# Performance work log

Measured on AMD Instinct MI355X. Metric: run time of the kernel, lower is better.

## Reference

```python
import jax, jax.numpy as jnp
import numpy as np

N_NODES = 100000
N_EDGES = 1600000
IN_DIM, HID_DIM, OUT_DIM = 128, 128, 1


def gcn_conv(x, W, b, src, dst, n_nodes):
    """PyG-style GCNConv: add self-loops, symmetric D^-1/2 (A+I) D^-1/2 normalization.

    x: [N, F_in], W: [F_in, F_out], b: [F_out], src/dst: [E] int edge endpoints.
    """
    h = x @ W  # [N, F_out] transform first (as PyG does)
    # degree on A + I, counted over destination (symmetric graph assumption)
    ones = jnp.ones(src.shape[0], dtype=h.dtype)
    deg = jax.ops.segment_sum(ones, dst, num_segments=n_nodes) + 1.0  # +1 self loop
    dinv = jax.lax.rsqrt(deg)  # [N]
    norm = dinv[src] * dinv[dst]  # [E] edge normalization
    msg = h[src] * norm[:, None]  # [E, F_out] gather + scale
    agg = jax.ops.segment_sum(msg, dst, num_segments=n_nodes)  # scatter-add
    # self-loop contribution: norm_ii = dinv[i]^2
    out = agg + h * (dinv * dinv)[:, None]
    return out + b


def setup_inputs() -> dict:
    key = jax.random.key(0)
    k1, k2, k3, k4 = jax.random.split(key, 4)
    x = jax.random.normal(k1, (N_NODES, IN_DIM), dtype=jnp.float32)
    edge_index = jax.random.randint(k2, (2, N_EDGES), 0, N_NODES, dtype=jnp.int64)
    W1 = jax.random.normal(k3, (IN_DIM, HID_DIM), dtype=jnp.float32) * (1.0 / np.sqrt(IN_DIM))
    b1 = jnp.zeros((HID_DIM,), dtype=jnp.float32)
    W2 = jax.random.normal(k4, (HID_DIM, OUT_DIM), dtype=jnp.float32) * (1.0 / np.sqrt(HID_DIM))
    b2 = jnp.zeros((OUT_DIM,), dtype=jnp.float32)
    return {"x": x, "edge_index": edge_index, "W1": W1, "b1": b1, "W2": W2, "b2": b2}


def reference(x, edge_index, W1, b1, W2, b2):
    n = x.shape[0]
    src, dst = edge_index[0], edge_index[1]
    h = gcn_conv(x, W1, b1, src, dst, n)
    h = jax.nn.relu(h)
    # dropout(p=0.2) is identity at inference
    out = gcn_conv(h, W2, b2, src, dst, n)  # [N, 1]
    return out
```

## Files before the change

kernel.cpp:

```cpp
#include <hip/hip_runtime.h>

#define N_NODES 100000
#define N_EDGES 1600000
#define DIM 128

#define BSHIFT 8
#define BNODES 256
#define NBUCK 391
#define BCAP  4608
#define PCHUNK 4096
#define NB_PART ((N_EDGES + PCHUNK - 1) / PCHUNK)

#define GTILES 1563

#define HALF_ELEMS ((size_t)N_NODES * 64)

typedef short s16x8 __attribute__((ext_vector_type(8)));
typedef float f32x4 __attribute__((ext_vector_type(4)));

__device__ __forceinline__ unsigned short f2bf(float f) {
    unsigned u = __float_as_uint(f);
    u += 0x7fffu + ((u >> 16) & 1u);
    return (unsigned short)(u >> 16);
}
__device__ __forceinline__ float bflo(unsigned u) { return __uint_as_float(u << 16); }
__device__ __forceinline__ float bfhi(unsigned u) { return __uint_as_float(u & 0xffff0000u); }

__device__ __forceinline__ void acc8(float (&a)[8], uint4 v, float w) {
    a[0] = fmaf(bflo(v.x), w, a[0]); a[1] = fmaf(bfhi(v.x), w, a[1]);
    a[2] = fmaf(bflo(v.y), w, a[2]); a[3] = fmaf(bfhi(v.y), w, a[3]);
    a[4] = fmaf(bflo(v.z), w, a[4]); a[5] = fmaf(bfhi(v.z), w, a[5]);
    a[6] = fmaf(bflo(v.w), w, a[6]); a[7] = fmaf(bfhi(v.w), w, a[7]);
}


__global__ void k_zero(int* __restrict__ gcur) {
    int t = blockIdx.x * blockDim.x + threadIdx.x;
    if (t < NBUCK) gcur[t] = t * BCAP;
}

__device__ __forceinline__ void part_body(char* smem, int bid,
                                          const int* __restrict__ src,
                                          const int* __restrict__ dst,
                                          int* __restrict__ gcur,
                                          int* __restrict__ ebuf) {
    int* hist = (int*)smem;
    int* gbase = hist + NBUCK;
    int tid = threadIdx.x;
    long e0 = (long)bid * PCHUNK;
    int n = min(PCHUNK, (int)(N_EDGES - e0));
    for (int b = tid; b < NBUCK; b += 256) hist[b] = 0;
    __syncthreads();

    int pk[16], mybk[16];
#pragma unroll
    for (int k = 0; k < 16; ++k) {
        int idx = k * 256 + tid;
        if (idx < n) {
            int s = src[e0 + idx], d = dst[e0 + idx];
            mybk[k] = d >> BSHIFT;
            pk[k] = (s << 8) | (d & 255);
            atomicAdd(&hist[mybk[k]], 1);
        } else {
            mybk[k] = -1;
        }
    }
    __syncthreads();
    for (int b = tid; b < NBUCK; b += 256) {
        gbase[b] = hist[b] ? atomicAdd(&gcur[b], hist[b]) : 0;
        hist[b] = 0;
    }
    __syncthreads();
#pragma unroll
    for (int k = 0; k < 16; ++k) {
        if (mybk[k] >= 0) {
            int b = mybk[k];
            int slot = gbase[b] + atomicAdd(&hist[b], 1);
            ebuf[slot] = pk[k];
        }
    }
}

__device__ __forceinline__ void csr_body(char* smem, int b,
                                         const int* __restrict__ ebuf,
                                         const int* __restrict__ gcur,
                                         int* __restrict__ rp,
                                         int* __restrict__ cnt,
                                         float* __restrict__ dinv,
                                         int* __restrict__ csrs) {
    int* lcnt = (int*)smem;
    int* lcur = lcnt + BNODES;
    int t = threadIdx.x;
    int node0 = b << BSHIFT;
    lcnt[t] = 0;
    __syncthreads();
    int base = b * BCAP, end = gcur[b];
    for (int e = base + t; e < end; e += 256)
        atomicAdd(&lcnt[ebuf[e] & 255], 1);
    __syncthreads();
    int c = lcnt[t];
    lcur[t] = c;
    __syncthreads();
    for (int s = 1; s < 256; s <<= 1) {
        int u = (t >= s) ? lcur[t - s] : 0;
        __syncthreads();
        lcur[t] += u;
        __syncthreads();
    }
    int excl = lcur[t] - c;
    lcur[t] = excl;
    int node = node0 + t;
    if (node < N_NODES) {
        rp[node] = base + excl;
        cnt[node] = c;
        dinv[node] = rsqrtf((float)(c + 1));
    }
    __syncthreads();
    for (int e = base + t; e < end; e += 256) {
        int pkd = ebuf[e];
        int p = atomicAdd(&lcur[pkd & 255], 1);
        csrs[base + p] = (int)((unsigned)pkd >> 8);
    }
}

__device__ __forceinline__ void gemm_body(char* smem, int tile,
                                          const float* __restrict__ x,
                                          const float* __restrict__ W1,
                                          unsigned short* __restrict__ h1h) {
    if (tile >= GTILES) return;
    unsigned short* Wt = (unsigned short*)smem;
    int tid = threadIdx.x;
    for (int idx = tid; idx < DIM * DIM; idx += 256) {
        int k = idx >> 7, c = idx & 127;
        Wt[c * 128 + (k ^ ((c & 7) << 3))] = f2bf(W1[idx]);
    }
    __syncthreads();

    int wv = tid >> 6, lane = tid & 63;
    int g = lane >> 4, tl = lane & 15;
    unsigned short* cst = (unsigned short*)(smem + 32768 + wv * 4096);

    int rb = tile * 64 + wv * 16;
    if (rb >= N_NODES) return;

    s16x8 afrag[4];
    const float* xrow = x + (size_t)(rb + tl) * DIM + g * 8;
#pragma unroll
    for (int kc = 0; kc < 4; ++kc) {
        float4 p0 = *(const float4*)(xrow + kc * 32);
        float4 p1 = *(const float4*)(xrow + kc * 32 + 4);
        s16x8 a;
        a[0] = (short)f2bf(p0.x); a[1] = (short)f2bf(p0.y);
        a[2] = (short)f2bf(p0.z); a[3] = (short)f2bf(p0.w);
        a[4] = (short)f2bf(p1.x); a[5] = (short)f2bf(p1.y);
        a[6] = (short)f2bf(p1.z); a[7] = (short)f2bf(p1.w);
        afrag[kc] = a;
    }

    f32x4 acc[8];
#pragma unroll
    for (int ct = 0; ct < 8; ++ct) acc[ct] = (f32x4)0.0f;
#pragma unroll
    for (int kc = 0; kc < 4; ++kc) {
#pragma unroll
        for (int ct = 0; ct < 8; ++ct) {
            int crow = ct * 16 + tl;
            int boff = crow * 256 + ((kc * 64 + g * 16) ^ ((crow & 7) << 4));
            s16x8 b = *(const s16x8*)((const char*)Wt + boff);
            acc[ct] = __builtin_amdgcn_mfma_f32_16x16x32_bf16(afrag[kc], b, acc[ct], 0, 0, 0);
        }
    }

#pragma unroll
    for (int ct = 0; ct < 8; ++ct) {
#pragma unroll
        for (int r = 0; r < 4; ++r) {
            float own = acc[ct][r];
            float oth = __shfl_xor(own, 1, 64);
            if ((lane & 1) == 0) {
                unsigned pk = (unsigned)f2bf(own) | ((unsigned)f2bf(oth) << 16);
                int row = g * 4 + r;
                int col = ct * 16 + tl;
                *(unsigned*)&cst[row * 128 + (col ^ (row << 3))] = pk;
            }
        }
    }
    asm volatile("s_waitcnt lgkmcnt(0)" ::: "memory");

    int hf = tl >> 3, ch = (tl & 7) * 8;
#pragma unroll
    for (int c = 0; c < 4; ++c) {
        int row = c * 4 + g;
        uint4 v = *(const uint4*)&cst[row * 128 + ((tl ^ row) * 8)];
        *(uint4*)(h1h + (size_t)hf * HALF_ELEMS + (size_t)(rb + row) * 64 + ch) = v;
    }
}

__global__ __launch_bounds__(256) void k_part(const int* __restrict__ src,
                                              const int* __restrict__ dst,
                                              int* __restrict__ gcur,
                                              int* __restrict__ ebuf) {
    __shared__ __align__(16) char smem[2 * NBUCK * 4 + 16];
    part_body(smem, blockIdx.x, src, dst, gcur, ebuf);
}

__global__ __launch_bounds__(256) void k_gemm(const float* __restrict__ x,
                                              const float* __restrict__ W1,
                                              unsigned short* __restrict__ h1h) {
    __shared__ __align__(16) char smem[49152];
    gemm_body(smem, blockIdx.x, x, W1, h1h);
}

__global__ __launch_bounds__(256) void k_csrk(const int* __restrict__ ebuf,
                                              const int* __restrict__ gcur,
                                              int* __restrict__ rp,
                                              int* __restrict__ cnt,
                                              float* __restrict__ dinv,
                                              int* __restrict__ csrs) {
    __shared__ __align__(16) char smem[2 * BNODES * 4];
    csr_body(smem, blockIdx.x, ebuf, gcur, rp, cnt, dinv, csrs);
}

__global__ __launch_bounds__(256) void k_pg(const int* __restrict__ src,
                                            const int* __restrict__ dst,
                                            int* __restrict__ gcur,
                                            int* __restrict__ ebuf,
                                            const float* __restrict__ x,
                                            const float* __restrict__ W1,
                                            unsigned short* __restrict__ h1h) {
    __shared__ __align__(16) char smem[49152];
    if (blockIdx.x < NB_PART) part_body(smem, blockIdx.x, src, dst, gcur, ebuf);
    else                      gemm_body(smem, blockIdx.x - NB_PART, x, W1, h1h);
}


__global__ __launch_bounds__(256) void k_agg1h(const unsigned short* __restrict__ h1h,
                                               const float* __restrict__ dinv,
                                               const int* __restrict__ rp,
                                               const int* __restrict__ cnt,
                                               const int* __restrict__ csrs,
                                               const float* __restrict__ b1,
                                               const float* __restrict__ W2,
                                               float* __restrict__ zpart) {
    int half = blockIdx.x & 1;
    int nb = blockIdx.x >> 1;
    int lane = threadIdx.x & 63;
    int wv = threadIdx.x >> 6;
    int g = lane >> 3, tl = lane & 7;
    int i = nb * 32 + wv * 8 + g;
    int c0 = tl * 8;
    const unsigned short* hbase = h1h + (size_t)half * HALF_ELEMS + c0;
    float di = dinv[i];
    int beg = rp[i], end = beg + cnt[i];
    float a[8];
#pragma unroll
    for (int q = 0; q < 8; ++q) a[q] = 0.f;

    int j = beg;
    for (; j + 4 <= end; j += 4) {
        int s0 = csrs[j], s1 = csrs[j + 1], s2 = csrs[j + 2], s3 = csrs[j + 3];
        uint4 v0 = *(const uint4*)(hbase + (size_t)s0 * 64);
        uint4 v1 = *(const uint4*)(hbase + (size_t)s1 * 64);
        uint4 v2 = *(const uint4*)(hbase + (size_t)s2 * 64);
        uint4 v3 = *(const uint4*)(hbase + (size_t)s3 * 64);
        float w0 = dinv[s0] * di, w1 = dinv[s1] * di;
        float w2 = dinv[s2] * di, w3 = dinv[s3] * di;
        acc8(a, v0, w0);
        acc8(a, v1, w1);
        acc8(a, v2, w2);
        acc8(a, v3, w3);
    }
    for (; j < end; ++j) {
        int s0 = csrs[j];
        uint4 v0 = *(const uint4*)(hbase + (size_t)s0 * 64);
        acc8(a, v0, dinv[s0] * di);
    }

    uint4 vs = *(const uint4*)(hbase + (size_t)i * 64);
    float sii = di * di;
    int cb = half * 64 + c0;
    float4 bA = *(const float4*)(b1 + cb);
    float4 bB = *(const float4*)(b1 + cb + 4);
    float4 wA = *(const float4*)(W2 + cb);
    float4 wB = *(const float4*)(W2 + cb + 4);
    float p = 0.f;
    p += fmaxf(fmaf(bflo(vs.x), sii, a[0]) + bA.x, 0.f) * wA.x;
    p += fmaxf(fmaf(bfhi(vs.x), sii, a[1]) + bA.y, 0.f) * wA.y;
    p += fmaxf(fmaf(bflo(vs.y), sii, a[2]) + bA.z, 0.f) * wA.z;
    p += fmaxf(fmaf(bfhi(vs.y), sii, a[3]) + bA.w, 0.f) * wA.w;
    p += fmaxf(fmaf(bflo(vs.z), sii, a[4]) + bB.x, 0.f) * wB.x;
    p += fmaxf(fmaf(bfhi(vs.z), sii, a[5]) + bB.y, 0.f) * wB.y;
    p += fmaxf(fmaf(bflo(vs.w), sii, a[6]) + bB.z, 0.f) * wB.z;
    p += fmaxf(fmaf(bfhi(vs.w), sii, a[7]) + bB.w, 0.f) * wB.w;
#pragma unroll
    for (int off = 4; off >= 1; off >>= 1) p += __shfl_xor(p, off, 64);
    if (tl == 0) zpart[(size_t)half * N_NODES + i] = p;
}


__global__ __launch_bounds__(256) void k_agg2(const float* __restrict__ zpart,
                                              const float* __restrict__ dinv,
                                              const int* __restrict__ rp,
                                              const int* __restrict__ cnt,
                                              const int* __restrict__ csrs,
                                              const float* __restrict__ b2,
                                              float* __restrict__ out) {
    int grp = threadIdx.x >> 2, r = threadIdx.x & 3;
    int i = blockIdx.x * 64 + grp;
    if (i >= N_NODES) return;
    float di = dinv[i];
    int beg = rp[i], end = beg + cnt[i];
    float acc = 0.f;
    for (int j = beg + r; j < end; j += 4) {
        int s = csrs[j];
        float zs = zpart[s] + zpart[N_NODES + s];
        acc = fmaf(zs, dinv[s] * di, acc);
    }
    acc += __shfl_xor(acc, 1, 64);
    acc += __shfl_xor(acc, 2, 64);
    if (r == 0) {
        float zi = zpart[i] + zpart[N_NODES + i];
        out[i] = acc + zi * di * di + b2[0];
    }
}


extern "C" void kernel_launch(void* const* d_in, const int* in_sizes, int n_in,
                              void* d_out, int out_size, void* d_ws, size_t ws_size,
                              hipStream_t stream) {
    const float* x  = (const float*)d_in[0];
    const int*   ei = (const int*)d_in[1];
    const float* W1 = (const float*)d_in[2];
    const float* b1 = (const float*)d_in[3];
    const float* W2 = (const float*)d_in[4];
    const float* b2 = (const float*)d_in[5];
    float* out = (float*)d_out;

    const int* src = ei;
    const int* dst = ei + N_EDGES;

    char* ws = (char*)d_ws;
    size_t o = 0;
    auto take = [&](size_t bytes) { char* p = ws + o; o += (bytes + 255) & ~(size_t)255; return p; };
    int*   cnt   = (int*)take(sizeof(int) * N_NODES);
    int*   rp    = (int*)take(sizeof(int) * N_NODES);
    int*   gcur  = (int*)take(sizeof(int) * (NBUCK + 1));
    float* dinv  = (float*)take(sizeof(float) * N_NODES);
    float* zpart = (float*)take(sizeof(float) * 2 * N_NODES);
    int*   csrs  = (int*)take(sizeof(int) * (size_t)NBUCK * BCAP);
    unsigned short* h1h = (unsigned short*)take(sizeof(unsigned short) * 2 * HALF_ELEMS);
    int* ebuf_sep = (int*)take(sizeof(int) * (size_t)NBUCK * BCAP);
    bool fused = (o <= ws_size);
    int* ebuf = fused ? ebuf_sep : (int*)h1h;

    k_zero<<<2, 256, 0, stream>>>(gcur);
    if (fused) {
        k_pg<<<NB_PART + GTILES, 256, 0, stream>>>(src, dst, gcur, ebuf, x, W1, h1h);
        k_csrk<<<NBUCK, 256, 0, stream>>>(ebuf, gcur, rp, cnt, dinv, csrs);
    } else {
        k_part<<<NB_PART, 256, 0, stream>>>(src, dst, gcur, ebuf);
        k_csrk<<<NBUCK, 256, 0, stream>>>(ebuf, gcur, rp, cnt, dinv, csrs);
        k_gemm<<<GTILES, 256, 0, stream>>>(x, W1, h1h);
    }
    k_agg1h<<<2 * (N_NODES / 32), 256, 0, stream>>>(h1h, dinv, rp, cnt, csrs, b1, W2, zpart);
    k_agg2<<<(N_NODES + 63) / 64, 256, 0, stream>>>(zpart, dinv, rp, cnt, csrs, b2, out);
}
```

Before: 143.9 us.

## Unfuse partition and GEMM kernels and halve the partition chunk size

Removes the combined partition+GEMM launch and always runs separate partition, CSR build and GEMM kernels. The partition kernel now uses only its small shared-memory histograms instead of inheriting the GEMM's 48KB allocation, which should allow more resident blocks. The edge chunk per partition block is halved, doubling block count and reducing per-thread register arrays, at the cost of more global atomics on bucket cursors. The trade-off is losing the overlap between GEMM tiles and edge partitioning, and paying one extra kernel launch.

```diff
diff --git a/kernel.cpp b/kernel.cpp
--- a/kernel.cpp
+++ b/kernel.cpp
@@ -8,7 +8,7 @@
 #define BNODES 256
 #define NBUCK 391
 #define BCAP  4608
-#define PCHUNK 4096
+#define PCHUNK 2048
 #define NB_PART ((N_EDGES + PCHUNK - 1) / PCHUNK)
 
 #define GTILES 1563
@@ -39,22 +39,21 @@
     if (t < NBUCK) gcur[t] = t * BCAP;
 }
 
-__device__ __forceinline__ void part_body(char* smem, int bid,
-                                          const int* __restrict__ src,
-                                          const int* __restrict__ dst,
-                                          int* __restrict__ gcur,
-                                          int* __restrict__ ebuf) {
-    int* hist = (int*)smem;
-    int* gbase = hist + NBUCK;
+__global__ __launch_bounds__(256) void k_part(const int* __restrict__ src,
+                                              const int* __restrict__ dst,
+                                              int* __restrict__ gcur,
+                                              int* __restrict__ ebuf) {
+    __shared__ int hist[NBUCK];
+    __shared__ int gbase[NBUCK];
     int tid = threadIdx.x;
-    long e0 = (long)bid * PCHUNK;
+    long e0 = (long)blockIdx.x * PCHUNK;
     int n = min(PCHUNK, (int)(N_EDGES - e0));
     for (int b = tid; b < NBUCK; b += 256) hist[b] = 0;
     __syncthreads();
 
-    int pk[16], mybk[16];
-#pragma unroll
-    for (int k = 0; k < 16; ++k) {
+    int pk[PCHUNK / 256], mybk[PCHUNK / 256];
+#pragma unroll
+    for (int k = 0; k < PCHUNK / 256; ++k) {
         int idx = k * 256 + tid;
         if (idx < n) {
             int s = src[e0 + idx], d = dst[e0 + idx];
@@ -72,7 +71,7 @@
     }
     __syncthreads();
 #pragma unroll
-    for (int k = 0; k < 16; ++k) {
+    for (int k = 0; k < PCHUNK / 256; ++k) {
         if (mybk[k] >= 0) {
             int b = mybk[k];
             int slot = gbase[b] + atomicAdd(&hist[b], 1);
@@ -81,16 +80,15 @@
     }
 }
 
-__device__ __forceinline__ void csr_body(char* smem, int b,
-                                         const int* __restrict__ ebuf,
-                                         const int* __restrict__ gcur,
-                                         int* __restrict__ rp,
-                                         int* __restrict__ cnt,
-                                         float* __restrict__ dinv,
-                                         int* __restrict__ csrs) {
-    int* lcnt = (int*)smem;
-    int* lcur = lcnt + BNODES;
-    int t = threadIdx.x;
+__global__ __launch_bounds__(256) void k_csrk(const int* __restrict__ ebuf,
+                                              const int* __restrict__ gcur,
+                                              int* __restrict__ rp,
+                                              int* __restrict__ cnt,
+                                              float* __restrict__ dinv,
+                                              int* __restrict__ csrs) {
+    __shared__ int lcnt[BNODES];
+    __shared__ int lcur[BNODES];
+    int b = blockIdx.x, t = threadIdx.x;
     int node0 = b << BSHIFT;
     lcnt[t] = 0;
     __syncthreads();
@@ -123,11 +121,11 @@
     }
 }
 
-__device__ __forceinline__ void gemm_body(char* smem, int tile,
-                                          const float* __restrict__ x,
-                                          const float* __restrict__ W1,
-                                          unsigned short* __restrict__ h1h) {
-    if (tile >= GTILES) return;
+__global__ __launch_bounds__(256) void k_gemm(const float* __restrict__ x,
+                                              const float* __restrict__ W1,
+                                              unsigned short* __restrict__ h1h) {
+    __shared__ __align__(16) char smem[49152];
+    int tile = blockIdx.x;
     unsigned short* Wt = (unsigned short*)smem;
     int tid = threadIdx.x;
     for (int idx = tid; idx < DIM * DIM; idx += 256) {
@@ -194,43 +192,6 @@
         uint4 v = *(const uint4*)&cst[row * 128 + ((tl ^ row) * 8)];
         *(uint4*)(h1h + (size_t)hf * HALF_ELEMS + (size_t)(rb + row) * 64 + ch) = v;
     }
-}
-
-__global__ __launch_bounds__(256) void k_part(const int* __restrict__ src,
-                                              const int* __restrict__ dst,
-                                              int* __restrict__ gcur,
-                                              int* __restrict__ ebuf) {
-    __shared__ __align__(16) char smem[2 * NBUCK * 4 + 16];
-    part_body(smem, blockIdx.x, src, dst, gcur, ebuf);
-}
-
-__global__ __launch_bounds__(256) void k_gemm(const float* __restrict__ x,
-                                              const float* __restrict__ W1,
-                                              unsigned short* __restrict__ h1h) {
-    __shared__ __align__(16) char smem[49152];
-    gemm_body(smem, blockIdx.x, x, W1, h1h);
-}
-
-__global__ __launch_bounds__(256) void k_csrk(const int* __restrict__ ebuf,
-                                              const int* __restrict__ gcur,
-                                              int* __restrict__ rp,
-                                              int* __restrict__ cnt,
-                                              float* __restrict__ dinv,
-                                              int* __restrict__ csrs) {
-    __shared__ __align__(16) char smem[2 * BNODES * 4];
-    csr_body(smem, blockIdx.x, ebuf, gcur, rp, cnt, dinv, csrs);
-}
-
-__global__ __launch_bounds__(256) void k_pg(const int* __restrict__ src,
-                                            const int* __restrict__ dst,
-                                            int* __restrict__ gcur,
-                                            int* __restrict__ ebuf,
-                                            const float* __restrict__ x,
-                                            const float* __restrict__ W1,
-                                            unsigned short* __restrict__ h1h) {
-    __shared__ __align__(16) char smem[49152];
-    if (blockIdx.x < NB_PART) part_body(smem, blockIdx.x, src, dst, gcur, ebuf);
-    else                      gemm_body(smem, blockIdx.x - NB_PART, x, W1, h1h);
 }
 
 
@@ -350,18 +311,13 @@
     int*   csrs  = (int*)take(sizeof(int) * (size_t)NBUCK * BCAP);
     unsigned short* h1h = (unsigned short*)take(sizeof(unsigned short) * 2 * HALF_ELEMS);
     int* ebuf_sep = (int*)take(sizeof(int) * (size_t)NBUCK * BCAP);
-    bool fused = (o <= ws_size);
-    int* ebuf = fused ? ebuf_sep : (int*)h1h;
+    bool sep = (o <= ws_size);
+    int* ebuf = sep ? ebuf_sep : (int*)h1h;
 
     k_zero<<<2, 256, 0, stream>>>(gcur);
-    if (fused) {
-        k_pg<<<NB_PART + GTILES, 256, 0, stream>>>(src, dst, gcur, ebuf, x, W1, h1h);
-        k_csrk<<<NBUCK, 256, 0, stream>>>(ebuf, gcur, rp, cnt, dinv, csrs);
-    } else {
-        k_part<<<NB_PART, 256, 0, stream>>>(src, dst, gcur, ebuf);
-        k_csrk<<<NBUCK, 256, 0, stream>>>(ebuf, gcur, rp, cnt, dinv, csrs);
-        k_gemm<<<GTILES, 256, 0, stream>>>(x, W1, h1h);
-    }
+    k_part<<<NB_PART, 256, 0, stream>>>(src, dst, gcur, ebuf);
+    k_csrk<<<NBUCK, 256, 0, stream>>>(ebuf, gcur, rp, cnt, dinv, csrs);
+    k_gemm<<<GTILES, 256, 0, stream>>>(x, W1, h1h);
     k_agg1h<<<2 * (N_NODES / 32), 256, 0, stream>>>(h1h, dinv, rp, cnt, csrs, b1, W2, zpart);
     k_agg2<<<(N_NODES + 63) / 64, 256, 0, stream>>>(zpart, dinv, rp, cnt, csrs, b2, out);
 }
```

Measured after the change: 163.9 us. +13.9%, slower.
